# Kernel optimization log

Hardware: AMD Instinct MI355X
Metric: run time of the kernel (lower is better)

The kernel has to match this reference:

```python
import jax, jax.numpy as jnp
import numpy as np

BN_EPS = 1e-5
NORM_EPS = 1e-12  # torch F.normalize eps


def setup_inputs() -> dict:
    key = jax.random.key(0)
    ks = jax.random.split(key, 7)
    B, N, D, K = 32, 4096, 512, 64
    init_sc = 1.0 / np.sqrt(D)
    x = jax.random.normal(ks[0], (B, N, D), dtype=jnp.float32)
    clusters = init_sc * jax.random.normal(ks[1], (D, K), dtype=jnp.float32)
    clusters2 = init_sc * jax.random.normal(ks[2], (1, D, K), dtype=jnp.float32)
    bn_weight = jax.random.uniform(ks[3], (K,), dtype=jnp.float32, minval=0.5, maxval=1.5)
    bn_bias = 0.1 * jax.random.normal(ks[4], (K,), dtype=jnp.float32)
    running_mean = 0.1 * jax.random.normal(ks[5], (K,), dtype=jnp.float32)
    running_var = jax.random.uniform(ks[6], (K,), dtype=jnp.float32, minval=0.5, maxval=1.5)
    return {"x": x, "clusters": clusters, "clusters2": clusters2,
            "bn_weight": bn_weight, "bn_bias": bn_bias,
            "running_mean": running_mean, "running_var": running_var}


def reference(x, clusters, clusters2, bn_weight, bn_bias, running_mean, running_var):
    B, N, D = x.shape
    K = clusters2.shape[2]
    x_flat = x.reshape(-1, D)                              # (B*N) x D
    logits = x_flat @ clusters                             # (B*N) x (K+G)
    # BatchNorm1d in eval mode: use running stats
    inv_std = jax.lax.rsqrt(running_var + BN_EPS)
    logits = (logits - running_mean) * inv_std * bn_weight + bn_bias
    assignment = jax.nn.softmax(logits, axis=1)[:, :K]     # drop ghost clusters
    assignment = assignment.reshape(B, N, K)
    a_sum = assignment.sum(axis=1, keepdims=True)
    a = a_sum * clusters2                                  # B x D x K
    vlad = jnp.einsum('bnk,bnd->bdk', assignment, x) - a   # B x D x K
    # intra-normalization over D (torch F.normalize dim=1)
    vlad = vlad / jnp.maximum(jnp.linalg.norm(vlad, axis=1, keepdims=True), NORM_EPS)
    vlad = vlad.reshape(B, D * K)
    vlad = vlad / jnp.maximum(jnp.linalg.norm(vlad, axis=1, keepdims=True), NORM_EPS)
    return vlad
```

## Files before the change

### kernel.cpp

```cpp
#include <hip/hip_runtime.h>
#include <stdint.h>

#define B_ 32
#define N_ 4096
#define D_ 512
#define K_ 64
#define M_ (B_ * N_)
#define NS 8
#define CPB 16

typedef float f32x4 __attribute__((ext_vector_type(4)));
typedef short bf16x8 __attribute__((ext_vector_type(8)));
typedef uint32_t u32;

union U8 { u32 u[4]; bf16x8 v; uint4 q4; };

__device__ __forceinline__ u32 pack_hi2(float a, float b) {
    return __builtin_amdgcn_perm(__float_as_uint(b), __float_as_uint(a), 0x07060302u);
}
__device__ __forceinline__ u32 lo16s(u32 p0, u32 p1) {
    return __builtin_amdgcn_perm(p1, p0, 0x05040100u);
}
__device__ __forceinline__ u32 hi16s(u32 p0, u32 p1) {
    return __builtin_amdgcn_perm(p1, p0, 0x07060302u);
}
__device__ __forceinline__ float trunc_hi(float f) {
    return __uint_as_float(__float_as_uint(f) & 0xffff0000u);
}

__device__ __forceinline__ void gload16(const void* g, void* l) {
    __builtin_amdgcn_global_load_lds(
        (const __attribute__((address_space(1))) u32*)g,
        (__attribute__((address_space(3))) u32*)l, 16, 0, 0);
}

__device__ __forceinline__ int xswb(int tok) {
    return ((tok & 7) ^ (tok >> 3)) << 4;
}

__device__ __forceinline__ void bar_lgkm() {
    asm volatile("s_waitcnt lgkmcnt(0)" ::: "memory");
    __builtin_amdgcn_sched_barrier(0);
    __builtin_amdgcn_s_barrier();
    __builtin_amdgcn_sched_barrier(0);
    asm volatile("" ::: "memory");
}

__global__ void k_prep(const float* __restrict__ clusters,
                       bf16x8* __restrict__ cfh, bf16x8* __restrict__ cfl)
{
    const int t = blockIdx.x;
    const int c = blockIdx.y;
    const int lane = threadIdx.x;
    const int q = lane >> 4, li = lane & 15;
    U8 h, l;
    #pragma unroll
    for (int j2 = 0; j2 < 4; ++j2) {
        float v0 = clusters[(t*32 + q*8 + 2*j2 + 0) * K_ + c*16 + li];
        float v1 = clusters[(t*32 + q*8 + 2*j2 + 1) * K_ + c*16 + li];
        float l0 = v0 - trunc_hi(v0), l1 = v1 - trunc_hi(v1);
        h.u[j2] = pack_hi2(v0, v1);
        l.u[j2] = pack_hi2(l0, l1);
    }
    cfh[(t*4 + c)*64 + lane] = h.v;
    cfl[(t*4 + c)*64 + lane] = l.v;
}

__global__ __launch_bounds__(256, 1) void k_fused(
    const float* __restrict__ x,
    const bf16x8* __restrict__ cfh, const bf16x8* __restrict__ cfl,
    const float* __restrict__ bnw, const float* __restrict__ bnb,
    const float* __restrict__ rm, const float* __restrict__ rv,
    float* __restrict__ part, float* __restrict__ a_sum)
{
    const int tid  = threadIdx.x;
    const int w    = tid >> 6, lane = tid & 63;
    const int q    = lane >> 4, li = lane & 15;
    const int s    = blockIdx.x, b = blockIdx.y;
    const size_t n0 = (size_t)b * N_ + (size_t)s * (N_ / NS);

    __shared__ __align__(16) float xt[2 * 32 * 512];
    __shared__ __align__(16) u32  at[64 * 32];
    __shared__ float red[32][4];

    const int col = w*16 + li;
    const float alpha = bnw[col] * rsqrtf(rv[col] + 1e-5f);
    const float beta  = bnb[col] - rm[col] * alpha;

    #pragma unroll
    for (int i = 0; i < 16; ++i) {
        const int off    = (w << 14) + (i << 10);
        const int tok    = off >> 11;
        const int within = (off & 2047) + (lane << 4);
        gload16((const char*)(x + (n0 + tok) * D_) + (within ^ xswb(tok)),
                (char*)xt + off);
    }

    bf16x8 cfh_r[16], cfl_r[16];
    #pragma unroll
    for (int t = 0; t < 16; ++t) {
        cfh_r[t] = cfh[(t*4 + w)*64 + lane];
        cfl_r[t] = cfl[(t*4 + w)*64 + lane];
    }

    f32x4 acc[4][8];
    #pragma unroll
    for (int i = 0; i < 4; ++i)
        #pragma unroll
        for (int j = 0; j < 8; ++j) acc[i][j] = (f32x4){0.f, 0.f, 0.f, 0.f};
    float rs = 0.f;

    __syncthreads();

    for (int ch = 0; ch < CPB; ++ch) {
        const int cur = ch & 1;
        const char* xb = (const char*)xt + cur * 65536;

        if (ch + 1 < CPB) {
            const size_t nbase = n0 + (size_t)(ch + 1) * 32;
            #pragma unroll
            for (int i = 0; i < 16; ++i) {
                const int off    = ((cur ^ 1) << 16) + (w << 14) + (i << 10);
                const int tok    = (off & 65535) >> 11;
                const int within = (off & 2047) + (lane << 4);
                gload16((const char*)(x + (nbase + tok) * D_) + (within ^ xswb(tok)),
                        (char*)xt + off);
            }
        }

        f32x4 lacc[2];
        lacc[0] = (f32x4){0.f,0.f,0.f,0.f};
        lacc[1] = (f32x4){0.f,0.f,0.f,0.f};
        #pragma unroll
        for (int t = 0; t < 16; ++t) {
            #pragma unroll
            for (int mt = 0; mt < 2; ++mt) {
                const int tokA = mt*16 + li;
                const char* xrow = xb + tokA * 2048;
                const int swbA = xswb(tokA);
                const int lin = t*128 + q*32;
                const uint4 r0 = *(const uint4*)(xrow + ( lin       ^ swbA));
                const uint4 r1 = *(const uint4*)(xrow + ((lin + 16) ^ swbA));
                float v[8];
                v[0]=__uint_as_float(r0.x); v[1]=__uint_as_float(r0.y);
                v[2]=__uint_as_float(r0.z); v[3]=__uint_as_float(r0.w);
                v[4]=__uint_as_float(r1.x); v[5]=__uint_as_float(r1.y);
                v[6]=__uint_as_float(r1.z); v[7]=__uint_as_float(r1.w);
                float lo[8];
                #pragma unroll
                for (int j = 0; j < 8; ++j) lo[j] = v[j] - trunc_hi(v[j]);
                U8 ah, al;
                #pragma unroll
                for (int j2 = 0; j2 < 4; ++j2) {
                    ah.u[j2] = pack_hi2(v[2*j2],  v[2*j2+1]);
                    al.u[j2] = pack_hi2(lo[2*j2], lo[2*j2+1]);
                }
                lacc[mt] = __builtin_amdgcn_mfma_f32_16x16x32_bf16(ah.v, cfh_r[t], lacc[mt], 0, 0, 0);
                lacc[mt] = __builtin_amdgcn_mfma_f32_16x16x32_bf16(ah.v, cfl_r[t], lacc[mt], 0, 0, 0);
                lacc[mt] = __builtin_amdgcn_mfma_f32_16x16x32_bf16(al.v, cfh_r[t], lacc[mt], 0, 0, 0);
            }
        }

        float er[2][4];
        #pragma unroll
        for (int mt = 0; mt < 2; ++mt)
            #pragma unroll
            for (int reg = 0; reg < 4; ++reg) {
                const float lg = fmaf(lacc[mt][reg], alpha, beta);
                const float e = __expf(lg);
                er[mt][reg] = e;
                float s0 = e;
                s0 += __shfl_xor(s0, 1);
                s0 += __shfl_xor(s0, 2);
                s0 += __shfl_xor(s0, 4);
                s0 += __shfl_xor(s0, 8);
                if (li == 0) red[mt*16 + q*4 + reg][w] = s0;
            }
        bar_lgkm();
        #pragma unroll
        for (int mt = 0; mt < 2; ++mt)
            #pragma unroll
            for (int reg = 0; reg < 4; ++reg) {
                const int tok = mt*16 + q*4 + reg;
                const float4 r4 = *(const float4*)&red[tok][0];
                const float inv = 1.0f / (r4.x + r4.y + r4.z + r4.w);
                const float a = er[mt][reg] * inv;
                rs += a;
                *(u32*)((char*)at + col*128 + ((tok*4) ^ ((col & 7) << 4))) =
                    pack_hi2(a, a - trunc_hi(a));
            }
        bar_lgkm();

        bf16x8 ah2[4], al2[4];
        #pragma unroll
        for (int mtv = 0; mtv < 4; ++mtv) {
            const int k = mtv*16 + li;
            const char* arow = (const char*)at + k*128;
            const int swb = (k & 7) << 4;
            const uint4 p0 = *(const uint4*)(arow + ((q*32)      ^ swb));
            const uint4 p1 = *(const uint4*)(arow + ((q*32 + 16) ^ swb));
            U8 uh, ul;
            uh.u[0] = lo16s(p0.x, p0.y); uh.u[1] = lo16s(p0.z, p0.w);
            uh.u[2] = lo16s(p1.x, p1.y); uh.u[3] = lo16s(p1.z, p1.w);
            ul.u[0] = hi16s(p0.x, p0.y); ul.u[1] = hi16s(p0.z, p0.w);
            ul.u[2] = hi16s(p1.x, p1.y); ul.u[3] = hi16s(p1.z, p1.w);
            ah2[mtv] = uh.v; al2[mtv] = ul.v;
        }
        const int d0 = w * 128;
        #pragma unroll
        for (int nt = 0; nt < 8; ++nt) {
            const int dcol = d0 + nt*16 + li;
            float v[8];
            #pragma unroll
            for (int j = 0; j < 8; ++j) {
                const int tok = q*8 + j;
                v[j] = *(const float*)(xb + tok*2048 + ((dcol*4) ^ xswb(tok)));
            }
            float lo[8];
            #pragma unroll
            for (int j = 0; j < 8; ++j) lo[j] = v[j] - trunc_hi(v[j]);
            U8 bh, bl;
            #pragma unroll
            for (int j2 = 0; j2 < 4; ++j2) {
                bh.u[j2] = pack_hi2(v[2*j2],  v[2*j2+1]);
                bl.u[j2] = pack_hi2(lo[2*j2], lo[2*j2+1]);
            }
            #pragma unroll
            for (int mtv = 0; mtv < 4; ++mtv) {
                acc[mtv][nt] = __builtin_amdgcn_mfma_f32_16x16x32_bf16(ah2[mtv], bh.v, acc[mtv][nt], 0, 0, 0);
                acc[mtv][nt] = __builtin_amdgcn_mfma_f32_16x16x32_bf16(ah2[mtv], bl.v, acc[mtv][nt], 0, 0, 0);
                acc[mtv][nt] = __builtin_amdgcn_mfma_f32_16x16x32_bf16(al2[mtv], bh.v, acc[mtv][nt], 0, 0, 0);
            }
        }
        __syncthreads();
    }

    float* pp = part + ((size_t)s * B_ + b) * ((size_t)K_ * D_);
    #pragma unroll
    for (int nt = 0; nt < 8; ++nt) {
        const int d = w*128 + nt*16 + li;
        #pragma unroll
        for (int mtv = 0; mtv < 4; ++mtv) {
            __builtin_nontemporal_store(acc[mtv][nt],
                (f32x4*)(pp + (size_t)d * K_ + mtv*16 + q*4));
        }
    }
    rs += __shfl_xor(rs, 16);
    rs += __shfl_xor(rs, 32);
    if (q == 0) atomicAdd(&a_sum[b*K_ + col], rs);
}

__global__ __launch_bounds__(256) void k_final1(
    const float* __restrict__ part_ro, const float* __restrict__ a_sum,
    const float* __restrict__ c2, float* __restrict__ part0,
    float* __restrict__ ssqk)
{
    const int b = blockIdx.x, dc = blockIdx.y;
    const int tid = threadIdx.x;
    const int w = tid >> 6, lane = tid & 63;
    const int q = lane >> 4, li = lane & 15;
    const int k4 = li * 4;
    const int d = dc*16 + w*4 + q;
    const size_t PS = (size_t)B_ * K_ * D_;
    const size_t base = (size_t)b * K_ * D_ + (size_t)d * K_ + k4;
    __shared__ float redk[4][64];

    float4 v = *(const float4*)(part_ro + base);
    #pragma unroll
    for (int ss = 1; ss < NS; ++ss) {
        const float4 p = *(const float4*)(part_ro + (size_t)ss*PS + base);
        v.x += p.x; v.y += p.y; v.z += p.z; v.w += p.w;
    }
    const float4 cv = *(const float4*)(c2 + (size_t)d * K_ + k4);
    const float4 av = *(const float4*)(a_sum + b*K_ + k4);
    v.x = fmaf(-av.x, cv.x, v.x);
    v.y = fmaf(-av.y, cv.y, v.y);
    v.z = fmaf(-av.z, cv.z, v.z);
    v.w = fmaf(-av.w, cv.w, v.w);
    *(float4*)(part0 + base) = v;

    float4 sq = make_float4(v.x*v.x, v.y*v.y, v.z*v.z, v.w*v.w);
    sq.x += __shfl_xor(sq.x, 16); sq.x += __shfl_xor(sq.x, 32);
    sq.y += __shfl_xor(sq.y, 16); sq.y += __shfl_xor(sq.y, 32);
    sq.z += __shfl_xor(sq.z, 16); sq.z += __shfl_xor(sq.z, 32);
    sq.w += __shfl_xor(sq.w, 16); sq.w += __shfl_xor(sq.w, 32);
    if (q == 0) *(float4*)&redk[w][k4] = sq;
    __syncthreads();
    if (tid < 64) {
        const float ssum = redk[0][tid] + redk[1][tid] + redk[2][tid] + redk[3][tid];
        atomicAdd(&ssqk[b*K_ + tid], ssum);
    }
}

__global__ __launch_bounds__(256) void k_final2(
    const float* __restrict__ v0, const float* __restrict__ ssqk,
    float* __restrict__ out)
{
    const int b = blockIdx.x, g = blockIdx.y;
    const int tid = threadIdx.x;
    __shared__ float invk[64];
    __shared__ float invg_s;

    if (tid < 64) {
        const float ss = ssqk[b*K_ + tid];
        const float inv = 1.0f / fmaxf(sqrtf(ss), 1e-12f);
        invk[tid] = inv;
        float gp = ss * inv * inv;
        #pragma unroll
        for (int m = 1; m < 64; m <<= 1) gp += __shfl_xor(gp, m);
        if (tid == 0) invg_s = 1.0f / fmaxf(sqrtf(gp), 1e-12f);
    }
    __syncthreads();

    const float ig = invg_s;
    const size_t bb = (size_t)b * K_ * D_;
    #pragma unroll
    for (int i = 0; i < 4; ++i) {
        const int f = g*1024 + i*256 + tid;
        const int k4 = (f & 15) * 4;
        const float4 v = *(const float4*)(v0 + bb + (size_t)f * 4);
        const float4 kv = *(const float4*)&invk[k4];
        float4 o;
        o.x = v.x * kv.x * ig;
        o.y = v.y * kv.y * ig;
        o.z = v.z * kv.z * ig;
        o.w = v.w * kv.w * ig;
        *(float4*)(out + bb + (size_t)f * 4) = o;
    }
}

extern "C" void kernel_launch(void* const* d_in, const int* in_sizes, int n_in,
                              void* d_out, int out_size, void* d_ws, size_t ws_size,
                              hipStream_t stream)
{
    const float* x    = (const float*)d_in[0];
    const float* clus = (const float*)d_in[1];
    const float* c2   = (const float*)d_in[2];
    const float* bnw  = (const float*)d_in[3];
    const float* bnb  = (const float*)d_in[4];
    const float* rm   = (const float*)d_in[5];
    const float* rv   = (const float*)d_in[6];
    float* out = (float*)d_out;

    float* part  = (float*)d_ws;
    float* a_sum = part + (size_t)NS * B_ * K_ * D_;
    float* ssqk  = a_sum + B_ * K_;
    bf16x8* cfh  = (bf16x8*)(ssqk + B_ * K_);
    bf16x8* cfl  = cfh + 16*4*64;

    hipMemsetAsync(a_sum, 0, 2 * B_ * K_ * sizeof(float), stream);

    k_prep<<<dim3(16, 4), 64, 0, stream>>>(clus, cfh, cfl);
    k_fused<<<dim3(NS, B_), 256, 0, stream>>>(x, cfh, cfl, bnw, bnb, rm, rv, part, a_sum);
    k_final1<<<dim3(B_, 32), 256, 0, stream>>>(part, a_sum, c2, part, ssqk);
    k_final2<<<dim3(B_, 8), 256, 0, stream>>>(part, ssqk, out);
}
```

Baseline: 440.2 us.

## Pre-split x into packed bf16 hi/lo in LDS via register loads, two blocks per CU

Replaces the async global-to-LDS double buffer with synchronous register loads that split each fp32 x value into bf16 hi/lo pairs once and store them packed in a single LDS buffer. Both GEMM stages then read the pre-split data with byte permutes instead of recomputing the split twice. LDS use is halved and launch bounds request two blocks per CU, with the N-split doubled (NS=16, CPB=8) to provide more blocks. The cost is losing the load/compute overlap of the prefetch pipeline, which now relies on the second resident block to hide latency, plus extra partial outputs to reduce.

```diff
diff --git a/kernel.cpp b/kernel.cpp
--- a/kernel.cpp
+++ b/kernel.cpp
@@ -6,8 +6,8 @@
 #define D_ 512
 #define K_ 64
 #define M_ (B_ * N_)
-#define NS 8
-#define CPB 16
+#define NS 16
+#define CPB 8
 
 typedef float f32x4 __attribute__((ext_vector_type(4)));
 typedef short bf16x8 __attribute__((ext_vector_type(8)));
@@ -28,22 +28,8 @@
     return __uint_as_float(__float_as_uint(f) & 0xffff0000u);
 }
 
-__device__ __forceinline__ void gload16(const void* g, void* l) {
-    __builtin_amdgcn_global_load_lds(
-        (const __attribute__((address_space(1))) u32*)g,
-        (__attribute__((address_space(3))) u32*)l, 16, 0, 0);
-}
-
-__device__ __forceinline__ int xswb(int tok) {
-    return ((tok & 7) ^ (tok >> 3)) << 4;
-}
-
-__device__ __forceinline__ void bar_lgkm() {
-    asm volatile("s_waitcnt lgkmcnt(0)" ::: "memory");
-    __builtin_amdgcn_sched_barrier(0);
-    __builtin_amdgcn_s_barrier();
-    __builtin_amdgcn_sched_barrier(0);
-    asm volatile("" ::: "memory");
+__device__ __forceinline__ int xswb2(int tok) {
+    return (((tok & 7) ^ (tok >> 3) ^ ((tok >> 3) << 2)) << 4);
 }
 
 __global__ void k_prep(const float* __restrict__ clusters,
@@ -66,7 +52,7 @@
     cfl[(t*4 + c)*64 + lane] = l.v;
 }
 
-__global__ __launch_bounds__(256, 1) void k_fused(
+__global__ __launch_bounds__(256, 2) void k_fused(
     const float* __restrict__ x,
     const bf16x8* __restrict__ cfh, const bf16x8* __restrict__ cfl,
     const float* __restrict__ bnw, const float* __restrict__ bnb,
@@ -79,23 +65,14 @@
     const int s    = blockIdx.x, b = blockIdx.y;
     const size_t n0 = (size_t)b * N_ + (size_t)s * (N_ / NS);
 
-    __shared__ __align__(16) float xt[2 * 32 * 512];
-    __shared__ __align__(16) u32  at[64 * 32];
+    __shared__ __align__(16) u32 xp[32 * 512];
+    __shared__ __align__(16) u32 at[64 * 36];
     __shared__ float red[32][4];
 
     const int col = w*16 + li;
     const float alpha = bnw[col] * rsqrtf(rv[col] + 1e-5f);
     const float beta  = bnb[col] - rm[col] * alpha;
 
-    #pragma unroll
-    for (int i = 0; i < 16; ++i) {
-        const int off    = (w << 14) + (i << 10);
-        const int tok    = off >> 11;
-        const int within = (off & 2047) + (lane << 4);
-        gload16((const char*)(x + (n0 + tok) * D_) + (within ^ xswb(tok)),
-                (char*)xt + off);
-    }
-
     bf16x8 cfh_r[16], cfl_r[16];
     #pragma unroll
     for (int t = 0; t < 16; ++t) {
@@ -109,24 +86,31 @@
         #pragma unroll
         for (int j = 0; j < 8; ++j) acc[i][j] = (f32x4){0.f, 0.f, 0.f, 0.f};
     float rs = 0.f;
-
-    __syncthreads();
+    const int qs = (q ^ (q << 2)) << 4;
 
     for (int ch = 0; ch < CPB; ++ch) {
-        const int cur = ch & 1;
-        const char* xb = (const char*)xt + cur * 65536;
-
-        if (ch + 1 < CPB) {
-            const size_t nbase = n0 + (size_t)(ch + 1) * 32;
-            #pragma unroll
-            for (int i = 0; i < 16; ++i) {
-                const int off    = ((cur ^ 1) << 16) + (w << 14) + (i << 10);
-                const int tok    = (off & 65535) >> 11;
-                const int within = (off & 2047) + (lane << 4);
-                gload16((const char*)(x + (nbase + tok) * D_) + (within ^ xswb(tok)),
-                        (char*)xt + off);
-            }
-        }
+        {
+            const size_t rbase = n0 + (size_t)ch * 32 + w * 8;
+            #pragma unroll
+            for (int half = 0; half < 2; ++half) {
+                float4 vv[8];
+                #pragma unroll
+                for (int rr = 0; rr < 8; ++rr)
+                    vv[rr] = *(const float4*)(x + (rbase + rr) * D_ + half*256 + lane*4);
+                #pragma unroll
+                for (int rr = 0; rr < 8; ++rr) {
+                    const int row = w*8 + rr;
+                    uint4 pq;
+                    pq.x = pack_hi2(vv[rr].x, vv[rr].x - trunc_hi(vv[rr].x));
+                    pq.y = pack_hi2(vv[rr].y, vv[rr].y - trunc_hi(vv[rr].y));
+                    pq.z = pack_hi2(vv[rr].z, vv[rr].z - trunc_hi(vv[rr].z));
+                    pq.w = pack_hi2(vv[rr].w, vv[rr].w - trunc_hi(vv[rr].w));
+                    *(uint4*)((char*)xp + row*2048 +
+                              ((half*1024 + lane*16) ^ xswb2(row))) = pq;
+                }
+            }
+        }
+        __syncthreads();
 
         f32x4 lacc[2];
         lacc[0] = (f32x4){0.f,0.f,0.f,0.f};
@@ -136,25 +120,16 @@
             #pragma unroll
             for (int mt = 0; mt < 2; ++mt) {
                 const int tokA = mt*16 + li;
-                const char* xrow = xb + tokA * 2048;
-                const int swbA = xswb(tokA);
+                const char* xrow = (const char*)xp + tokA * 2048;
+                const int swbA = xswb2(tokA);
                 const int lin = t*128 + q*32;
-                const uint4 r0 = *(const uint4*)(xrow + ( lin       ^ swbA));
-                const uint4 r1 = *(const uint4*)(xrow + ((lin + 16) ^ swbA));
-                float v[8];
-                v[0]=__uint_as_float(r0.x); v[1]=__uint_as_float(r0.y);
-                v[2]=__uint_as_float(r0.z); v[3]=__uint_as_float(r0.w);
-                v[4]=__uint_as_float(r1.x); v[5]=__uint_as_float(r1.y);
-                v[6]=__uint_as_float(r1.z); v[7]=__uint_as_float(r1.w);
-                float lo[8];
-                #pragma unroll
-                for (int j = 0; j < 8; ++j) lo[j] = v[j] - trunc_hi(v[j]);
+                const uint4 p0 = *(const uint4*)(xrow + ( lin       ^ swbA));
+                const uint4 p1 = *(const uint4*)(xrow + ((lin + 16) ^ swbA));
                 U8 ah, al;
-                #pragma unroll
-                for (int j2 = 0; j2 < 4; ++j2) {
-                    ah.u[j2] = pack_hi2(v[2*j2],  v[2*j2+1]);
-                    al.u[j2] = pack_hi2(lo[2*j2], lo[2*j2+1]);
-                }
+                ah.u[0] = lo16s(p0.x, p0.y); ah.u[1] = lo16s(p0.z, p0.w);
+                ah.u[2] = lo16s(p1.x, p1.y); ah.u[3] = lo16s(p1.z, p1.w);
+                al.u[0] = hi16s(p0.x, p0.y); al.u[1] = hi16s(p0.z, p0.w);
+                al.u[2] = hi16s(p1.x, p1.y); al.u[3] = hi16s(p1.z, p1.w);
                 lacc[mt] = __builtin_amdgcn_mfma_f32_16x16x32_bf16(ah.v, cfh_r[t], lacc[mt], 0, 0, 0);
                 lacc[mt] = __builtin_amdgcn_mfma_f32_16x16x32_bf16(ah.v, cfl_r[t], lacc[mt], 0, 0, 0);
                 lacc[mt] = __builtin_amdgcn_mfma_f32_16x16x32_bf16(al.v, cfh_r[t], lacc[mt], 0, 0, 0);
@@ -176,9 +151,10 @@
                 s0 += __shfl_xor(s0, 8);
                 if (li == 0) red[mt*16 + q*4 + reg][w] = s0;
             }
-        bar_lgkm();
-        #pragma unroll
-        for (int mt = 0; mt < 2; ++mt)
+        __syncthreads();
+        #pragma unroll
+        for (int mt = 0; mt < 2; ++mt) {
+            u32 prr[4];
             #pragma unroll
             for (int reg = 0; reg < 4; ++reg) {
                 const int tok = mt*16 + q*4 + reg;
@@ -186,19 +162,19 @@
                 const float inv = 1.0f / (r4.x + r4.y + r4.z + r4.w);
                 const float a = er[mt][reg] * inv;
                 rs += a;
-                *(u32*)((char*)at + col*128 + ((tok*4) ^ ((col & 7) << 4))) =
-                    pack_hi2(a, a - trunc_hi(a));
-            }
-        bar_lgkm();
+                prr[reg] = pack_hi2(a, a - trunc_hi(a));
+            }
+            *(uint4*)((char*)at + col*144 + (mt*16 + q*4)*4) =
+                make_uint4(prr[0], prr[1], prr[2], prr[3]);
+        }
+        __syncthreads();
 
         bf16x8 ah2[4], al2[4];
         #pragma unroll
         for (int mtv = 0; mtv < 4; ++mtv) {
-            const int k = mtv*16 + li;
-            const char* arow = (const char*)at + k*128;
-            const int swb = (k & 7) << 4;
-            const uint4 p0 = *(const uint4*)(arow + ((q*32)      ^ swb));
-            const uint4 p1 = *(const uint4*)(arow + ((q*32 + 16) ^ swb));
+            const char* arow = (const char*)at + (mtv*16 + li)*144 + q*32;
+            const uint4 p0 = *(const uint4*)(arow);
+            const uint4 p1 = *(const uint4*)(arow + 16);
             U8 uh, ul;
             uh.u[0] = lo16s(p0.x, p0.y); uh.u[1] = lo16s(p0.z, p0.w);
             uh.u[2] = lo16s(p1.x, p1.y); uh.u[3] = lo16s(p1.z, p1.w);
@@ -206,25 +182,20 @@
             ul.u[2] = hi16s(p1.x, p1.y); ul.u[3] = hi16s(p1.z, p1.w);
             ah2[mtv] = uh.v; al2[mtv] = ul.v;
         }
-        const int d0 = w * 128;
+        const char* xq = (const char*)xp + q * 16384;
         #pragma unroll
         for (int nt = 0; nt < 8; ++nt) {
-            const int dcol = d0 + nt*16 + li;
-            float v[8];
-            #pragma unroll
-            for (int j = 0; j < 8; ++j) {
-                const int tok = q*8 + j;
-                v[j] = *(const float*)(xb + tok*2048 + ((dcol*4) ^ xswb(tok)));
-            }
-            float lo[8];
-            #pragma unroll
-            for (int j = 0; j < 8; ++j) lo[j] = v[j] - trunc_hi(v[j]);
+            const int dcol = w*128 + nt*16 + li;
+            const int e = (dcol*4) ^ qs;
+            u32 p[8];
+            #pragma unroll
+            for (int j = 0; j < 8; ++j)
+                p[j] = *(const u32*)(xq + j*2048 + (e ^ (j << 4)));
             U8 bh, bl;
-            #pragma unroll
-            for (int j2 = 0; j2 < 4; ++j2) {
-                bh.u[j2] = pack_hi2(v[2*j2],  v[2*j2+1]);
-                bl.u[j2] = pack_hi2(lo[2*j2], lo[2*j2+1]);
-            }
+            bh.u[0] = lo16s(p[0], p[1]); bh.u[1] = lo16s(p[2], p[3]);
+            bh.u[2] = lo16s(p[4], p[5]); bh.u[3] = lo16s(p[6], p[7]);
+            bl.u[0] = hi16s(p[0], p[1]); bl.u[1] = hi16s(p[2], p[3]);
+            bl.u[2] = hi16s(p[4], p[5]); bl.u[3] = hi16s(p[6], p[7]);
             #pragma unroll
             for (int mtv = 0; mtv < 4; ++mtv) {
                 acc[mtv][nt] = __builtin_amdgcn_mfma_f32_16x16x32_bf16(ah2[mtv], bh.v, acc[mtv][nt], 0, 0, 0);
```

New measurement: 634.3 us. 1.44x slower.
